# Kernel optimization log

Measured on AMD Instinct MI355X. Metric: run time of the kernel, lower is better.

Reference implementation:

```python
import jax, jax.numpy as jnp
import numpy as np

B, S, D = 4, 4096, 2048
SCAN, STATE = 128, 16


def setup_inputs() -> dict:
    key = jax.random.key(0)
    ks = jax.random.split(key, 8)
    scale = 1.0 / np.sqrt(D)
    scale_s = 1.0 / np.sqrt(SCAN)
    x = jax.random.normal(ks[0], (B, S, D), dtype=jnp.float32)
    Wi = jax.random.normal(ks[1], (SCAN, D), dtype=jnp.float32) * scale
    Wo = jax.random.normal(ks[2], (D, SCAN), dtype=jnp.float32) * 0.02  # torch zero-inits; small random for nontrivial output
    A_log = jax.random.normal(ks[3], (SCAN, STATE), dtype=jnp.float32) * 0.1
    Wb = jax.random.normal(ks[4], (STATE, SCAN), dtype=jnp.float32) * scale_s
    Wc = jax.random.normal(ks[5], (STATE, SCAN), dtype=jnp.float32) * scale_s
    Wdt = jax.random.normal(ks[6], (SCAN, SCAN), dtype=jnp.float32) * scale_s
    b_dt = jnp.full((SCAN,), -3.0, dtype=jnp.float32)
    Wg = jax.random.normal(ks[7], (SCAN, D), dtype=jnp.float32) * scale
    return {"x": x, "Wi": Wi, "Wo": Wo, "A_log": A_log, "Wb": Wb,
            "Wc": Wc, "Wdt": Wdt, "b_dt": b_dt, "Wg": Wg}


def _selective_scan_ffn(x, Wi, Wo, A_log, Wb, Wc, Wdt, b_dt, Wg):
    z = jnp.einsum('bsd,nd->bsn', x, Wi)                      # [B,S,SCAN]
    gate = jax.nn.silu(jnp.einsum('bsd,nd->bsn', x, Wg))      # [B,S,SCAN]
    A = -jnp.exp(A_log)                                        # [SCAN,STATE]
    B_in = jnp.einsum('bsn,kn->bsk', z, Wb)                   # [B,S,STATE]
    C_in = jnp.einsum('bsn,kn->bsk', z, Wc)                   # [B,S,STATE]
    dt = jax.nn.softplus(jnp.einsum('bsn,mn->bsm', z, Wdt) + b_dt)  # [B,S,SCAN]
    A_bar = 1.0 + dt[..., None] * A                            # [B,S,SCAN,STATE]

    def step(state, inp):
        a_t, dt_t, z_t, b_t, c_t = inp
        # state: [B,SCAN,STATE]
        state = a_t * state + dt_t[..., None] * (z_t[..., None] * b_t[:, None, :])
        y = jnp.einsum('bnk,bk->bn', state, c_t)               # [B,SCAN]
        return state, y

    xs = (jnp.moveaxis(A_bar, 1, 0), jnp.moveaxis(dt, 1, 0),
          jnp.moveaxis(z, 1, 0), jnp.moveaxis(B_in, 1, 0), jnp.moveaxis(C_in, 1, 0))
    state0 = jnp.zeros((x.shape[0], Wi.shape[0], A_log.shape[1]), dtype=x.dtype)
    _, ys = jax.lax.scan(step, state0, xs)                     # [S,B,SCAN]
    y = jnp.moveaxis(ys, 0, 1) * gate                          # [B,S,SCAN]
    return jnp.einsum('bsn,dn->bsd', y, Wo)                    # [B,S,D]


def reference(x, Wi, Wo, A_log, Wb, Wc, Wdt, b_dt, Wg):
    return _selective_scan_ffn(x, Wi, Wo, A_log, Wb, Wc, Wdt, b_dt, Wg)
```

## Files before the change

### kernel.cpp

```cpp
#include <hip/hip_runtime.h>
#include <hip/hip_bf16.h>
#include <math.h>

using bf16 = __hip_bfloat16;
typedef __attribute__((ext_vector_type(8))) short bf16x8;
typedef __attribute__((ext_vector_type(8))) short short8;
typedef __attribute__((ext_vector_type(4))) float f32x4;

#define AS1 __attribute__((address_space(1)))
#define AS3 __attribute__((address_space(3)))

constexpr int BATCH = 4;
constexpr int SEQ   = 4096;
constexpr int DIM   = 2048;
constexpr int SCAN  = 128;
constexpr int STATE = 16;
constexpr int LCH   = 16;
constexpr int NCH   = SEQ / LCH;

__device__ __forceinline__ float bf2f(bf16 v) { return __bfloat162float(v); }
__device__ __forceinline__ bf16  f2bf(float v) { return __float2bfloat16(v); }
__device__ __forceinline__ float bfbits(unsigned short u) {
  return __uint_as_float((unsigned)u << 16);
}

__device__ __forceinline__ int probe_dtype(const unsigned short* __restrict__ xp) {
  int cnt = 0;
  for (int i = 0; i < 512; ++i) {
    int e = (xp[i] >> 7) & 0xFF;
    cnt += (e >= 107 && e <= 147) ? 1 : 0;
  }
  return (cnt >= 410) ? 1 : 0;
}

__device__ __forceinline__ void conv_b(const void* src, bf16* dst, int n, int f,
                                       int gtid, int nt) {
  if (f) { const bf16* s = (const bf16*)src;  for (int i = gtid; i < n; i += nt) dst[i] = s[i]; }
  else   { const float* s = (const float*)src; for (int i = gtid; i < n; i += nt) dst[i] = f2bf(s[i]); }
}
__device__ __forceinline__ void conv_f(const void* src, float* dst, int n, int f,
                                       int gtid, int nt) {
  if (f) { const bf16* s = (const bf16*)src;  for (int i = gtid; i < n; i += nt) dst[i] = bf2f(s[i]); }
  else   { const float* s = (const float*)src; for (int i = gtid; i < n; i += nt) dst[i] = s[i]; }
}
__device__ __forceinline__ void conv_aneg(const void* src, float* dst, int n, int f,
                                          int gtid, int nt) {
  if (f) { const bf16* s = (const bf16*)src;  for (int i = gtid; i < n; i += nt) dst[i] = -expf(bf2f(s[i])); }
  else   { const float* s = (const float*)src; for (int i = gtid; i < n; i += nt) dst[i] = -expf(s[i]); }
}

__global__ __launch_bounds__(256) void kconv_w(
    const unsigned short* __restrict__ xprobe,
    const void* Wi, const void* Wg, const void* Wo, const void* Wdt,
    const void* Wb, const void* Wc, const void* bdt, const void* Alog,
    bf16* Wzg, bf16* Wob, bf16* Wdtb, bf16* Wbb, bf16* Wcb,
    float* bdtf, float* Anegf, int* __restrict__ flag) {
  int f = probe_dtype(xprobe);
  if (blockIdx.x == 0 && threadIdx.x == 0) *flag = f;
  int nt = gridDim.x * blockDim.x;
  int g  = blockIdx.x * blockDim.x + threadIdx.x;
  conv_b(Wi,  Wzg,               SCAN * DIM,  f, g, nt);
  conv_b(Wg,  Wzg + SCAN * DIM,  SCAN * DIM,  f, g, nt);
  conv_b(Wo,  Wob,  DIM * SCAN,  f, g, nt);
  conv_b(Wdt, Wdtb, SCAN * SCAN, f, g, nt);
  conv_b(Wb,  Wbb,  STATE * SCAN, f, g, nt);
  conv_b(Wc,  Wcb,  STATE * SCAN, f, g, nt);
  conv_f(bdt,  bdtf,  SCAN,          f, g, nt);
  conv_aneg(Alog, Anegf, SCAN * STATE, f, g, nt);
}

__device__ __forceinline__ int swzb(int row, int colbyte) {
  return row * 128 + (colbyte ^ ((row & 7) << 4));
}

struct ARegs { float4 v[2]; };

template <int F>
__device__ __forceinline__ ARegs loadA(const void* __restrict__ xin, size_t rowbase,
                                       int k0, int ae) {
  ARegs r;
  if (F) {
    r.v[0] = *(const float4*)((const bf16*)xin + rowbase + k0 + ae);
  } else {
    const float4* s = (const float4*)((const float*)xin + rowbase + k0 + ae);
    r.v[0] = s[0]; r.v[1] = s[1];
  }
  return r;
}

template <int F>
__device__ __forceinline__ void writeA(char* abuf, int ar, int ae, const ARegs& rg) {
  char* d = abuf + swzb(ar, ae * 2);
  if (F) {
    *(float4*)d = rg.v[0];
  } else {
    union { short8 s; bf16 b[8]; } u;
    const float* fv = (const float*)&rg.v[0];
#pragma unroll
    for (int i = 0; i < 8; ++i) u.b[i] = f2bf(fv[i]);
    *(short8*)d = u.s;
  }
}

__device__ __forceinline__ void stageB(const bf16* __restrict__ W, int k0,
                                       char* bbuf, int tid) {
  int w = tid >> 6;
#pragma unroll
  for (int i = 0; i < 4; ++i) {
    int off = i * 8192 + tid * 16;
    int r   = off >> 7;
    int cbl = off & 127;
    int cbs = cbl ^ ((r & 7) << 4);
    const bf16* src = W + (size_t)r * DIM + k0 + (cbs >> 1);
    char* lb = bbuf + i * 8192 + w * 1024;
    __builtin_amdgcn_global_load_lds((const AS1 void*)src, (AS3 void*)lb, 16, 0, 0);
  }
}

__device__ __forceinline__ void compute64x256_8w(const char* abuf, const char* bbuf,
                                                 int tid, f32x4 acc[4][2]) {
  int l = tid & 63, w = tid >> 6;
  int wc = w * 32;
  int lr = l & 15, lk = (l >> 4) * 8;
#pragma unroll
  for (int kk = 0; kk < 64; kk += 32) {
    int cb = (kk + lk) * 2;
    bf16x8 a[4], b[2];
#pragma unroll
    for (int m = 0; m < 4; ++m)
      a[m] = *(const bf16x8*)(abuf + swzb(m * 16 + lr, cb));
#pragma unroll
    for (int n = 0; n < 2; ++n)
      b[n] = *(const bf16x8*)(bbuf + swzb(wc + n * 16 + lr, cb));
#pragma unroll
    for (int m = 0; m < 4; ++m)
#pragma unroll
      for (int n = 0; n < 2; ++n)
        acc[m][n] = __builtin_amdgcn_mfma_f32_16x16x32_bf16(a[m], b[n], acc[m][n], 0, 0, 0);
  }
}

__device__ __forceinline__ void vm_wait6() { asm volatile("s_waitcnt vmcnt(6)" ::: "memory"); __builtin_amdgcn_sched_barrier(0); }
__device__ __forceinline__ void vm_wait5() { asm volatile("s_waitcnt vmcnt(5)" ::: "memory"); __builtin_amdgcn_sched_barrier(0); }
__device__ __forceinline__ void vm_wait0() { asm volatile("s_waitcnt vmcnt(0)" ::: "memory"); __builtin_amdgcn_sched_barrier(0); }
__device__ __forceinline__ void lgkm0_barrier() {
  asm volatile("s_waitcnt lgkmcnt(0)" ::: "memory");
  __builtin_amdgcn_sched_barrier(0);
  __builtin_amdgcn_s_barrier();
}

template <int F>
__device__ __forceinline__ void k1_main(const void* __restrict__ xin,
                                        const bf16* __restrict__ W,
                                        char* lds, size_t xrow, int ar, int ae,
                                        int tid, f32x4 acc[4][2]) {
  constexpr int NK = DIM / 64;
  constexpr int BUF = 40960;
  ARegs aH = loadA<F>(xin, xrow, 0, ae);
  stageB(W, 0, lds + 0 * BUF + 8192, tid);
  ARegs aN = loadA<F>(xin, xrow, 64, ae);
  stageB(W, 64, lds + 1 * BUF + 8192, tid);
  if (F) vm_wait5(); else vm_wait6();
  writeA<F>(lds + 0 * BUF, ar, ae, aH);
  aH = aN;
  lgkm0_barrier();

  for (int t = 0; t < NK; ++t) {
    char* curb = lds + (t % 3) * BUF;
    if (t + 2 < NK) {
      aN = loadA<F>(xin, xrow, (t + 2) * 64, ae);
      stageB(W, (t + 2) * 64, lds + ((t + 2) % 3) * BUF + 8192, tid);
    }
    compute64x256_8w(curb, curb + 8192, tid, acc);
    if (t + 1 < NK) {
      if (t + 2 < NK) { if (F) vm_wait5(); else vm_wait6(); }
      else            { vm_wait0(); }
      writeA<F>(lds + ((t + 1) % 3) * BUF, ar, ae, aH);
      aH = aN;
      lgkm0_barrier();
    }
  }
}

__global__ __launch_bounds__(512) void k12_zg(const void* __restrict__ xin,
                                              const bf16* __restrict__ Wzg,
                                              const bf16* __restrict__ Wdtb,
                                              const bf16* __restrict__ Wbb,
                                              const bf16* __restrict__ Wcb,
                                              const float* __restrict__ bdtf,
                                              const float* __restrict__ Aneg,
                                              bf16* __restrict__ z,
                                              bf16* __restrict__ gate,
                                              float* __restrict__ dt,
                                              float* __restrict__ Bv,
                                              float* __restrict__ Cv,
                                              float* __restrict__ fin,
                                              float* __restrict__ apr,
                                              const int* __restrict__ flag) {
  __shared__ char lds[122880];
  int tid = threadIdx.x;
  int mb  = blockIdx.x;
  int m0  = mb * 64;
  int f   = *flag;
  int ar  = tid >> 3;
  int ae  = (tid & 7) * 8;
  size_t xrow = ((size_t)m0 + ar) * DIM;

  f32x4 acc[4][2];
#pragma unroll
  for (int m = 0; m < 4; ++m)
#pragma unroll
    for (int n = 0; n < 2; ++n)
#pragma unroll
      for (int j = 0; j < 4; ++j) acc[m][n][j] = 0.f;

  if (f) k1_main<1>(xin, Wzg, lds, xrow, ar, ae, tid, acc);
  else   k1_main<0>(xin, Wzg, lds, xrow, ar, ae, tid, acc);

  __syncthreads();

  bf16 (*zl)[128]   = (bf16 (*)[128])(lds);
  bf16 (*wl)[136]   = (bf16 (*)[136])(lds + 16384);
  bf16 (*dtlb)[128] = (bf16 (*)[128])(lds + 59904);
  bf16 (*Blcb)[16]  = (bf16 (*)[16]) (lds + 76288);

  {
    int l = tid & 63, w = tid >> 6;
    int wcg = w * 32;
    int sel = w >> 2;
    int cb  = (w & 3) * 32;
    int lr = l & 15, lj = (l >> 4) * 4;
    bf16* o = sel ? gate : z;
#pragma unroll
    for (int m = 0; m < 4; ++m)
#pragma unroll
      for (int n = 0; n < 2; ++n)
#pragma unroll
        for (int j = 0; j < 4; ++j) {
          int rowl = m * 16 + lj + j;
          int col  = cb + n * 16 + lr;
          float v = acc[m][n][j];
          if (sel) v = v / (1.f + expf(-v));
          bf16 bv = f2bf(v);
          o[(size_t)(m0 + rowl) * SCAN + col] = bv;
          if (!sel) zl[rowl][col] = bv;
        }
    (void)wcg;
  }
  for (int idx = tid; idx < 160 * 16; idx += 512) {
    int r = idx >> 4, c8 = (idx & 15) << 3;
    const bf16* src;
    if (r < 128)      src = Wdtb + r * 128;
    else if (r < 144) src = Wbb + (r - 128) * 128;
    else              src = Wcb + (r - 144) * 128;
    *(short8*)&wl[r][c8] = *(const short8*)(src + c8);
  }
  __syncthreads();

  if (tid < 256) {
    int l = tid & 63, w = tid >> 6;
    int lr = l & 15, lk = (l >> 4) * 8, lj = (l >> 4) * 4;
    f32x4 acc2[10];
#pragma unroll
    for (int n = 0; n < 10; ++n)
#pragma unroll
      for (int j = 0; j < 4; ++j) acc2[n][j] = 0.f;

#pragma unroll
    for (int kk = 0; kk < 128; kk += 32) {
      bf16x8 a = *(const bf16x8*)&zl[w * 16 + lr][kk + lk];
#pragma unroll
      for (int n = 0; n < 10; ++n) {
        bf16x8 bfr = *(const bf16x8*)&wl[n * 16 + lr][kk + lk];
        acc2[n] = __builtin_amdgcn_mfma_f32_16x16x32_bf16(a, bfr, acc2[n], 0, 0, 0);
      }
    }

#pragma unroll
    for (int n = 0; n < 10; ++n) {
      int o = n * 16 + lr;
#pragma unroll
      for (int j = 0; j < 4; ++j) {
        int row = w * 16 + lj + j;
        float v = acc2[n][j];
        if (o < 128) {
          v += bdtf[o];
          v = fmaxf(v, 0.f) + log1pf(expf(-fabsf(v)));
          dt[(size_t)(m0 + row) * SCAN + o] = v;
          dtlb[row][o] = f2bf(v);
        } else if (o < 144) {
          Bv[(size_t)(m0 + row) * STATE + (o - 128)] = v;
          Blcb[row][o - 128] = f2bf(v);
        } else {
          Cv[(size_t)(m0 + row) * STATE + (o - 144)] = v;
        }
      }
    }
  }
  __syncthreads();

  {
    int n  = tid & 127;
    int cc = tid >> 7;
    int b   = m0 >> 12;
    int ch0 = (m0 & 4095) >> 4;
    float A[STATE];
#pragma unroll
    for (int k = 0; k < STATE; ++k) A[k] = Aneg[n * STATE + k];

    float st[STATE], ap[STATE];
#pragma unroll
    for (int k = 0; k < STATE; ++k) { st[k] = 0.f; ap[k] = 1.f; }
#pragma unroll
    for (int t = 0; t < LCH; ++t) {
      int row = cc * LCH + t;
      float d = bf2f(dtlb[row][n]);
      float u = d * bf2f(zl[row][n]);
#pragma unroll
      for (int kg = 0; kg < 4; ++kg) {
        unsigned long long bb = *(const unsigned long long*)&Blcb[row][kg * 4];
        float b0 = bfbits((unsigned short)bb);
        float b1 = bfbits((unsigned short)(bb >> 16));
        float b2 = bfbits((unsigned short)(bb >> 32));
        float b3 = bfbits((unsigned short)(bb >> 48));
        float a;
        a = fmaf(d, A[kg*4+0], 1.f); st[kg*4+0] = fmaf(a, st[kg*4+0], u * b0); ap[kg*4+0] *= a;
        a = fmaf(d, A[kg*4+1], 1.f); st[kg*4+1] = fmaf(a, st[kg*4+1], u * b1); ap[kg*4+1] *= a;
        a = fmaf(d, A[kg*4+2], 1.f); st[kg*4+2] = fmaf(a, st[kg*4+2], u * b2); ap[kg*4+2] *= a;
        a = fmaf(d, A[kg*4+3], 1.f); st[kg*4+3] = fmaf(a, st[kg*4+3], u * b3); ap[kg*4+3] *= a;
      }
    }
    size_t base = ((size_t)b * NCH + (ch0 + cc)) * (STATE * SCAN) + n;
#pragma unroll
    for (int k = 0; k < STATE; ++k) {
      fin[base + k * SCAN] = st[k];
      apr[base + k * SCAN] = ap[k];
    }
  }
}

__global__ __launch_bounds__(64) void k3b(const float* __restrict__ fin,
                                          float* __restrict__ apr) {
  int c  = blockIdx.x * 64 + threadIdx.x;
  int b  = c >> 11;
  int kn = c & 2047;
  size_t base = (size_t)b * NCH * 2048 + kn;
  float s = 0.f;
  for (int g = 0; g < NCH; g += 16) {
    float fv[16], av[16];
#pragma unroll
    for (int i = 0; i < 16; ++i) {
      size_t o = base + (size_t)(g + i) * 2048;
      fv[i] = fin[o];
      av[i] = apr[o];
    }
#pragma unroll
    for (int i = 0; i < 16; ++i) {
      size_t o = base + (size_t)(g + i) * 2048;
      apr[o] = s;
      s = fmaf(av[i], s, fv[i]);
    }
  }
}

__global__ __launch_bounds__(128) void k3c(
    const float* __restrict__ dt, const bf16* z,
    const float* __restrict__ Bv, const float* __restrict__ Cv,
    const float* __restrict__ Aneg, const float* __restrict__ inc,
    const bf16* __restrict__ gate, bf16* yg) {
  __shared__ float Bl[LCH][STATE];
  __shared__ float Cl[LCH][STATE];
  int n  = threadIdx.x;
  int ch = blockIdx.x, b = blockIdx.y;
  int t0 = ch * LCH;
  if (n < LCH * STATE / 4)
    ((float4*)&Bl[0][0])[n] = ((const float4*)(Bv + ((size_t)b * SEQ + t0) * STATE))[n];
  else if (n < LCH * STATE / 2)
    ((float4*)&Cl[0][0])[n - LCH * STATE / 4] =
        ((const float4*)(Cv + ((size_t)b * SEQ + t0) * STATE))[n - LCH * STATE / 4];

  size_t base = ((size_t)b * NCH + ch) * (STATE * SCAN) + n;
  float A[STATE], st[STATE];
#pragma unroll
  for (int k = 0; k < STATE; ++k) {
    A[k]  = Aneg[n * STATE + k];
    st[k] = inc[base + k * SCAN];
  }
  __syncthreads();

  const float* dtp = dt   + ((size_t)b * SEQ + t0) * SCAN + n;
  const bf16*  zp  = z    + ((size_t)b * SEQ + t0) * SCAN + n;
  const bf16*  gp  = gate + ((size_t)b * SEQ + t0) * SCAN + n;
  bf16*        yp  = yg   + ((size_t)b * SEQ + t0) * SCAN + n;
#pragma unroll 4
  for (int t = 0; t < LCH; ++t) {
    float d = dtp[t * SCAN];
    float u = d * bf2f(zp[t * SCAN]);
    float g = bf2f(gp[t * SCAN]);
    float y0 = 0.f, y1 = 0.f, y2 = 0.f, y3 = 0.f;
#pragma unroll
    for (int kg = 0; kg < 4; ++kg) {
      float4 B4 = *(const float4*)&Bl[t][kg * 4];
      float4 C4 = *(const float4*)&Cl[t][kg * 4];
      float a, p = 0.f;
      a = fmaf(d, A[kg*4+0], 1.f); st[kg*4+0] = fmaf(a, st[kg*4+0], u * B4.x); p = fmaf(st[kg*4+0], C4.x, p);
      a = fmaf(d, A[kg*4+1], 1.f); st[kg*4+1] = fmaf(a, st[kg*4+1], u * B4.y); p = fmaf(st[kg*4+1], C4.y, p);
      a = fmaf(d, A[kg*4+2], 1.f); st[kg*4+2] = fmaf(a, st[kg*4+2], u * B4.z); p = fmaf(st[kg*4+2], C4.z, p);
      a = fmaf(d, A[kg*4+3], 1.f); st[kg*4+3] = fmaf(a, st[kg*4+3], u * B4.w); p = fmaf(st[kg*4+3], C4.w, p);
      if (kg == 0) y0 = p; else if (kg == 1) y1 = p; else if (kg == 2) y2 = p; else y3 = p;
    }
    float y = (y0 + y1) + (y2 + y3);
    yp[t * SCAN] = f2bf(y * g);
  }
}

__device__ __forceinline__ int swz256(int row, int colbyte) {
  return row * 256 + (colbyte ^ ((row & 7) << 4));
}

__global__ __launch_bounds__(256) void k4_out(const bf16* __restrict__ yg,
                                              const bf16* __restrict__ Wo,
                                              void* __restrict__ outv,
                                              const int* __restrict__ flag) {
  __shared__ char lds[49152];
  int tid = threadIdx.x;
  int mb = blockIdx.x, nb = blockIdx.y;
  int w = tid >> 6;

#pragma unroll
  for (int i = 0; i < 8; ++i) {
    int off = i * 4096 + tid * 16;
    int r   = off >> 8;
    int cbl = off & 255;
    int cbs = cbl ^ ((r & 7) << 4);
    const bf16* src = yg + (size_t)(mb * 128 + r) * SCAN + (cbs >> 1);
    __builtin_amdgcn_global_load_lds((const AS1 void*)src,
                                     (AS3 void*)(lds + i * 4096 + w * 1024), 16, 0, 0);
  }
#pragma unroll
  for (int i = 0; i < 4; ++i) {
    int off = i * 4096 + tid * 16;
    int r   = off >> 8;
    int cbl = off & 255;
    int cbs = cbl ^ ((r & 7) << 4);
    const bf16* src = Wo + (size_t)(nb * 64 + r) * SCAN + (cbs >> 1);
    __builtin_amdgcn_global_load_lds((const AS1 void*)src,
                                     (AS3 void*)(lds + 32768 + i * 4096 + w * 1024), 16, 0, 0);
  }
  __syncthreads();

  int l = tid & 63;
  int lr = l & 15, lk = (l >> 4) * 8;
  f32x4 acc[2][4];
#pragma unroll
  for (int m = 0; m < 2; ++m)
#pragma unroll
    for (int n = 0; n < 4; ++n)
#pragma unroll
      for (int j = 0; j < 4; ++j) acc[m][n][j] = 0.f;

#pragma unroll
  for (int kk = 0; kk < 128; kk += 32) {
    int cb = (kk + lk) * 2;
    bf16x8 a[2], b[4];
#pragma unroll
    for (int m = 0; m < 2; ++m)
      a[m] = *(const bf16x8*)(lds + swz256(w * 32 + m * 16 + lr, cb));
#pragma unroll
    for (int n = 0; n < 4; ++n)
      b[n] = *(const bf16x8*)(lds + 32768 + swz256(n * 16 + lr, cb));
#pragma unroll
    for (int m = 0; m < 2; ++m)
#pragma unroll
      for (int n = 0; n < 4; ++n)
        acc[m][n] = __builtin_amdgcn_mfma_f32_16x16x32_bf16(a[m], b[n], acc[m][n], 0, 0, 0);
  }

  int f = *flag;
  int lj = (l >> 4) * 4;
#pragma unroll
  for (int m = 0; m < 2; ++m)
#pragma unroll
    for (int n = 0; n < 4; ++n)
#pragma unroll
      for (int j = 0; j < 4; ++j) {
        int row = mb * 128 + w * 32 + m * 16 + lj + j;
        int col = nb * 64 + n * 16 + lr;
        size_t off = (size_t)row * DIM + col;
        float v = acc[m][n][j];
        if (f) ((bf16*)outv)[off] = f2bf(v);
        else   ((float*)outv)[off] = v;
      }
}

extern "C" void kernel_launch(void* const* d_in, const int* in_sizes, int n_in,
                              void* d_out, int out_size, void* d_ws, size_t ws_size,
                              hipStream_t stream) {
  const void* x     = d_in[0];
  const void* Wi    = d_in[1];
  const void* Wo    = d_in[2];
  const void* A_log = d_in[3];
  const void* Wb    = d_in[4];
  const void* Wc    = d_in[5];
  const void* Wdt   = d_in[6];
  const void* b_dt  = d_in[7];
  const void* Wg    = d_in[8];

  const size_t M = (size_t)BATCH * SEQ;
  char* p = (char*)d_ws;
  int*   flag = (int*)p;    p += 256;
  bf16*  Wzg  = (bf16*)p;   p += (size_t)2 * SCAN * DIM * 2;
  bf16*  Wob  = (bf16*)p;   p += (size_t)DIM * SCAN * 2;
  bf16*  Wdtb = (bf16*)p;   p += (size_t)SCAN * SCAN * 2;
  bf16*  Wbb  = (bf16*)p;   p += (size_t)STATE * SCAN * 2;
  bf16*  Wcb  = (bf16*)p;   p += (size_t)STATE * SCAN * 2;
  float* bdtf = (float*)p;  p += SCAN * 4;
  float* Anegf= (float*)p;  p += (size_t)SCAN * STATE * 4;
  bf16*  z    = (bf16*)p;   p += M * SCAN * 2;
  bf16*  gate = (bf16*)p;   p += M * SCAN * 2;
  bf16*  yg   = z;
  float* dt   = (float*)p;  p += M * SCAN * 4;
  float* Bv   = (float*)p;  p += M * STATE * 4;
  float* Cv   = (float*)p;  p += M * STATE * 4;
  float* fin  = (float*)p;  p += (size_t)BATCH * NCH * SCAN * STATE * 4;
  float* apr  = (float*)p;  p += (size_t)BATCH * NCH * SCAN * STATE * 4;

  kconv_w <<<256, 256, 0, stream>>>((const unsigned short*)x,
                                    Wi, Wg, Wo, Wdt, Wb, Wc, b_dt, A_log,
                                    Wzg, Wob, Wdtb, Wbb, Wcb, bdtf, Anegf, flag);
  k12_zg  <<<dim3(256), 512, 0, stream>>>(x, Wzg, Wdtb, Wbb, Wcb, bdtf, Anegf,
                                          z, gate, dt, Bv, Cv, fin, apr, flag);
  k3b     <<<dim3(128), 64, 0, stream>>>(fin, apr);
  k3c     <<<dim3(NCH, BATCH), 128, 0, stream>>>(dt, z, Bv, Cv, Anegf, apr, gate, yg);
  k4_out  <<<dim3(128, 32), 256, 0, stream>>>(yg, Wob, d_out, flag);
}
```

Measured before the change: 145.5 us.

## Run fused z/gate GEMM kernel with 16 waves per block instead of 8

The fused input-projection kernel now launches 1024 threads per block. Its 64x256 output tile is split across 16 waves in a 2x8 layout, so each wave computes a 32x32 sub-tile instead of 64x32. Per-thread A and B staging loads are halved and the vmcnt waits are retuned to match. The later phases are adjusted to the new thread count, with the chunk-scan section limited to the first 512 threads. The aim is more latency hiding and memory parallelism on a grid of only 256 blocks. The cost is fewer registers per thread, more barrier participants, and smaller, less efficient global loads.

```diff
diff --git a/kernel.cpp b/kernel.cpp
--- a/kernel.cpp
+++ b/kernel.cpp
@@ -5,6 +5,7 @@
 using bf16 = __hip_bfloat16;
 typedef __attribute__((ext_vector_type(8))) short bf16x8;
 typedef __attribute__((ext_vector_type(8))) short short8;
+typedef __attribute__((ext_vector_type(4))) short short4v;
 typedef __attribute__((ext_vector_type(4))) float f32x4;
 
 #define AS1 __attribute__((address_space(1)))
@@ -73,17 +74,17 @@
   return row * 128 + (colbyte ^ ((row & 7) << 4));
 }
 
-struct ARegs { float4 v[2]; };
+struct ARegs { float4 v; };
 
 template <int F>
 __device__ __forceinline__ ARegs loadA(const void* __restrict__ xin, size_t rowbase,
                                        int k0, int ae) {
   ARegs r;
   if (F) {
-    r.v[0] = *(const float4*)((const bf16*)xin + rowbase + k0 + ae);
+    float2 t = *(const float2*)((const bf16*)xin + rowbase + k0 + ae);
+    r.v.x = t.x; r.v.y = t.y; r.v.z = 0.f; r.v.w = 0.f;
   } else {
-    const float4* s = (const float4*)((const float*)xin + rowbase + k0 + ae);
-    r.v[0] = s[0]; r.v[1] = s[1];
+    r.v = *(const float4*)((const float*)xin + rowbase + k0 + ae);
   }
   return r;
 }
@@ -92,13 +93,12 @@
 __device__ __forceinline__ void writeA(char* abuf, int ar, int ae, const ARegs& rg) {
   char* d = abuf + swzb(ar, ae * 2);
   if (F) {
-    *(float4*)d = rg.v[0];
+    *(float2*)d = make_float2(rg.v.x, rg.v.y);
   } else {
-    union { short8 s; bf16 b[8]; } u;
-    const float* fv = (const float*)&rg.v[0];
-#pragma unroll
-    for (int i = 0; i < 8; ++i) u.b[i] = f2bf(fv[i]);
-    *(short8*)d = u.s;
+    union { float2 f2; bf16 b[4]; } u;
+    u.b[0] = f2bf(rg.v.x); u.b[1] = f2bf(rg.v.y);
+    u.b[2] = f2bf(rg.v.z); u.b[3] = f2bf(rg.v.w);
+    *(float2*)d = u.f2;
   }
 }
 
@@ -106,42 +106,42 @@
                                        char* bbuf, int tid) {
   int w = tid >> 6;
 #pragma unroll
-  for (int i = 0; i < 4; ++i) {
-    int off = i * 8192 + tid * 16;
+  for (int i = 0; i < 2; ++i) {
+    int off = i * 16384 + tid * 16;
     int r   = off >> 7;
     int cbl = off & 127;
     int cbs = cbl ^ ((r & 7) << 4);
     const bf16* src = W + (size_t)r * DIM + k0 + (cbs >> 1);
-    char* lb = bbuf + i * 8192 + w * 1024;
+    char* lb = bbuf + i * 16384 + w * 1024;
     __builtin_amdgcn_global_load_lds((const AS1 void*)src, (AS3 void*)lb, 16, 0, 0);
   }
 }
 
-__device__ __forceinline__ void compute64x256_8w(const char* abuf, const char* bbuf,
-                                                 int tid, f32x4 acc[4][2]) {
+__device__ __forceinline__ void compute64x256_16w(const char* abuf, const char* bbuf,
+                                                  int tid, f32x4 acc[2][2]) {
   int l = tid & 63, w = tid >> 6;
-  int wc = w * 32;
+  int wr = (w >> 3) * 32;
+  int wc = (w & 7) * 32;
   int lr = l & 15, lk = (l >> 4) * 8;
 #pragma unroll
   for (int kk = 0; kk < 64; kk += 32) {
     int cb = (kk + lk) * 2;
-    bf16x8 a[4], b[2];
-#pragma unroll
-    for (int m = 0; m < 4; ++m)
-      a[m] = *(const bf16x8*)(abuf + swzb(m * 16 + lr, cb));
+    bf16x8 a[2], b[2];
+#pragma unroll
+    for (int m = 0; m < 2; ++m)
+      a[m] = *(const bf16x8*)(abuf + swzb(wr + m * 16 + lr, cb));
 #pragma unroll
     for (int n = 0; n < 2; ++n)
       b[n] = *(const bf16x8*)(bbuf + swzb(wc + n * 16 + lr, cb));
 #pragma unroll
-    for (int m = 0; m < 4; ++m)
+    for (int m = 0; m < 2; ++m)
 #pragma unroll
       for (int n = 0; n < 2; ++n)
         acc[m][n] = __builtin_amdgcn_mfma_f32_16x16x32_bf16(a[m], b[n], acc[m][n], 0, 0, 0);
   }
 }
 
-__device__ __forceinline__ void vm_wait6() { asm volatile("s_waitcnt vmcnt(6)" ::: "memory"); __builtin_amdgcn_sched_barrier(0); }
-__device__ __forceinline__ void vm_wait5() { asm volatile("s_waitcnt vmcnt(5)" ::: "memory"); __builtin_amdgcn_sched_barrier(0); }
+__device__ __forceinline__ void vm_wait3() { asm volatile("s_waitcnt vmcnt(3)" ::: "memory"); __builtin_amdgcn_sched_barrier(0); }
 __device__ __forceinline__ void vm_wait0() { asm volatile("s_waitcnt vmcnt(0)" ::: "memory"); __builtin_amdgcn_sched_barrier(0); }
 __device__ __forceinline__ void lgkm0_barrier() {
   asm volatile("s_waitcnt lgkmcnt(0)" ::: "memory");
@@ -153,14 +153,14 @@
 __device__ __forceinline__ void k1_main(const void* __restrict__ xin,
                                         const bf16* __restrict__ W,
                                         char* lds, size_t xrow, int ar, int ae,
-                                        int tid, f32x4 acc[4][2]) {
+                                        int tid, f32x4 acc[2][2]) {
   constexpr int NK = DIM / 64;
   constexpr int BUF = 40960;
   ARegs aH = loadA<F>(xin, xrow, 0, ae);
   stageB(W, 0, lds + 0 * BUF + 8192, tid);
   ARegs aN = loadA<F>(xin, xrow, 64, ae);
   stageB(W, 64, lds + 1 * BUF + 8192, tid);
-  if (F) vm_wait5(); else vm_wait6();
+  vm_wait3();
   writeA<F>(lds + 0 * BUF, ar, ae, aH);
   aH = aN;
   lgkm0_barrier();
@@ -171,10 +171,10 @@
       aN = loadA<F>(xin, xrow, (t + 2) * 64, ae);
       stageB(W, (t + 2) * 64, lds + ((t + 2) % 3) * BUF + 8192, tid);
     }
-    compute64x256_8w(curb, curb + 8192, tid, acc);
+    compute64x256_16w(curb, curb + 8192, tid, acc);
     if (t + 1 < NK) {
-      if (t + 2 < NK) { if (F) vm_wait5(); else vm_wait6(); }
-      else            { vm_wait0(); }
+      if (t + 2 < NK) vm_wait3();
+      else            vm_wait0();
       writeA<F>(lds + ((t + 1) % 3) * BUF, ar, ae, aH);
       aH = aN;
       lgkm0_barrier();
@@ -182,33 +182,33 @@
   }
 }
 
-__global__ __launch_bounds__(512) void k12_zg(const void* __restrict__ xin,
-                                              const bf16* __restrict__ Wzg,
-                                              const bf16* __restrict__ Wdtb,
-                                              const bf16* __restrict__ Wbb,
-                                              const bf16* __restrict__ Wcb,
-                                              const float* __restrict__ bdtf,
-                                              const float* __restrict__ Aneg,
-                                              bf16* __restrict__ z,
-                                              bf16* __restrict__ gate,
-                                              float* __restrict__ dt,
-                                              float* __restrict__ Bv,
-                                              float* __restrict__ Cv,
-                                              float* __restrict__ fin,
-                                              float* __restrict__ apr,
-                                              const int* __restrict__ flag) {
+__global__ __launch_bounds__(1024) void k12_zg(const void* __restrict__ xin,
+                                               const bf16* __restrict__ Wzg,
+                                               const bf16* __restrict__ Wdtb,
+                                               const bf16* __restrict__ Wbb,
+                                               const bf16* __restrict__ Wcb,
+                                               const float* __restrict__ bdtf,
+                                               const float* __restrict__ Aneg,
+                                               bf16* __restrict__ z,
+                                               bf16* __restrict__ gate,
+                                               float* __restrict__ dt,
+                                               float* __restrict__ Bv,
+                                               float* __restrict__ Cv,
+                                               float* __restrict__ fin,
+                                               float* __restrict__ apr,
+                                               const int* __restrict__ flag) {
   __shared__ char lds[122880];
   int tid = threadIdx.x;
   int mb  = blockIdx.x;
   int m0  = mb * 64;
   int f   = *flag;
-  int ar  = tid >> 3;
-  int ae  = (tid & 7) * 8;
+  int ar  = tid >> 4;
+  int ae  = (tid & 15) * 4;
   size_t xrow = ((size_t)m0 + ar) * DIM;
 
-  f32x4 acc[4][2];
-#pragma unroll
-  for (int m = 0; m < 4; ++m)
+  f32x4 acc[2][2];
+#pragma unroll
+  for (int m = 0; m < 2; ++m)
 #pragma unroll
     for (int n = 0; n < 2; ++n)
 #pragma unroll
@@ -226,18 +226,19 @@
 
   {
     int l = tid & 63, w = tid >> 6;
-    int wcg = w * 32;
-    int sel = w >> 2;
-    int cb  = (w & 3) * 32;
+    int wr = (w >> 3) * 32;
+    int wcg = (w & 7) * 32;
+    int sel = wcg >> 7;
+    int cb  = wcg & 127;
     int lr = l & 15, lj = (l >> 4) * 4;
     bf16* o = sel ? gate : z;
 #pragma unroll
-    for (int m = 0; m < 4; ++m)
+    for (int m = 0; m < 2; ++m)
 #pragma unroll
       for (int n = 0; n < 2; ++n)
 #pragma unroll
         for (int j = 0; j < 4; ++j) {
-          int rowl = m * 16 + lj + j;
+          int rowl = wr + m * 16 + lj + j;
           int col  = cb + n * 16 + lr;
           float v = acc[m][n][j];
           if (sel) v = v / (1.f + expf(-v));
@@ -245,9 +246,8 @@
           o[(size_t)(m0 + rowl) * SCAN + col] = bv;
           if (!sel) zl[rowl][col] = bv;
         }
-    (void)wcg;
-  }
-  for (int idx = tid; idx < 160 * 16; idx += 512) {
+  }
+  for (int idx = tid; idx < 160 * 16; idx += 1024) {
     int r = idx >> 4, c8 = (idx & 15) << 3;
     const bf16* src;
     if (r < 128)      src = Wdtb + r * 128;
@@ -299,7 +299,7 @@
   }
   __syncthreads();
 
-  {
+  if (tid < 512) {
     int n  = tid & 127;
     int cc = tid >> 7;
     int b   = m0 >> 12;
@@ -528,8 +528,8 @@
   kconv_w <<<256, 256, 0, stream>>>((const unsigned short*)x,
                                     Wi, Wg, Wo, Wdt, Wb, Wc, b_dt, A_log,
                                     Wzg, Wob, Wdtb, Wbb, Wcb, bdtf, Anegf, flag);
-  k12_zg  <<<dim3(256), 512, 0, stream>>>(x, Wzg, Wdtb, Wbb, Wcb, bdtf, Anegf,
-                                          z, gate, dt, Bv, Cv, fin, apr, flag);
+  k12_zg  <<<dim3(256), 1024, 0, stream>>>(x, Wzg, Wdtb, Wbb, Wcb, bdtf, Anegf,
+                                           z, gate, dt, Bv, Cv, fin, apr, flag);
   k3b     <<<dim3(128), 64, 0, stream>>>(fin, apr);
   k3c     <<<dim3(NCH, BATCH), 128, 0, stream>>>(dt, z, Bv, Cv, Anegf, apr, gate, yg);
   k4_out  <<<dim3(128, 32), 256, 0, stream>>>(yg, Wob, d_out, flag);
```

New measurement: 139.9 us. 3.9% less time.
